# Kernel tuning notes

Measured on AMD Instinct MI355X. Metric: run time of the kernel, lower is better.

The kernel has to match this reference:

```python
import jax, jax.numpy as jnp
import numpy as np

LN_EPS = 1e-5


def layernorm(x, g, b):
    mu = jnp.mean(x, axis=-1, keepdims=True)
    var = jnp.mean((x - mu) ** 2, axis=-1, keepdims=True)
    return (x - mu) * jax.lax.rsqrt(var + LN_EPS) * g + b


def attention(x, qkv_w, proj_w, proj_b, num_heads):
    B, N, C = x.shape
    d = C // num_heads
    qkv = jnp.einsum('bnc,oc->bno', x, qkv_w)            # [B,N,3C], no bias (qkv_bias=False)
    qkv = qkv.reshape(B, N, num_heads, 3 * d).transpose(0, 2, 1, 3)  # [B,h,N,3d]
    q, k, v = qkv[..., :d], qkv[..., d:2 * d], qkv[..., 2 * d:]
    scores = jnp.einsum('bhnd,bhmd->bhnm', q, k) * (d ** -0.5)
    a = jax.nn.softmax(scores, axis=-1)
    o = jnp.einsum('bhnm,bhmd->bhnd', a, v).transpose(0, 2, 1, 3).reshape(B, N, C)
    return jnp.einsum('bnc,oc->bno', o, proj_w) + proj_b


def dwconv(x, w, b, H, W):
    # x: [B,N,C] -> NCHW depthwise 3x3 conv, stride 1, pad 1 -> [B,N,C]
    B, N, C = x.shape
    xi = x.transpose(0, 2, 1).reshape(B, C, H, W)
    y = jax.lax.conv_general_dilated(
        xi, w, window_strides=(1, 1), padding='SAME',
        dimension_numbers=('NCHW', 'OIHW', 'NCHW'), feature_group_count=C)
    y = y + b[None, :, None, None]
    return y.reshape(B, C, H * W).transpose(0, 2, 1)


def mlp(x, fc1_w, fc1_b, dw_w, dw_b, fc2_w, fc2_b, H, W):
    h = jnp.einsum('bnc,oc->bno', x, fc1_w) + fc1_b
    h = dwconv(h, dw_w, dw_b, H, W)
    h = jax.nn.gelu(h, approximate=False)  # torch nn.GELU default = exact erf
    return jnp.einsum('bnh,oh->bno', h, fc2_w) + fc2_b


def setup_inputs() -> dict:
    key = jax.random.key(0)
    ks = jax.random.split(key, 8)
    B, N, C, HID = 8, 1024, 512, 2048
    s = 0.02
    return {
        'x': jax.random.normal(ks[0], (B, N, C), jnp.float32),
        'ln1_g': jnp.ones((C,), jnp.float32),
        'ln1_b': jnp.zeros((C,), jnp.float32),
        'qkv_w': jax.random.normal(ks[1], (3 * C, C), jnp.float32) * s,
        'proj_w': jax.random.normal(ks[2], (C, C), jnp.float32) * s,
        'proj_b': jnp.zeros((C,), jnp.float32),
        'ln2_g': jnp.ones((C,), jnp.float32),
        'ln2_b': jnp.zeros((C,), jnp.float32),
        'fc1_w': jax.random.normal(ks[3], (HID, C), jnp.float32) * s,
        'fc1_b': jnp.zeros((HID,), jnp.float32),
        'dw_w': jax.random.normal(ks[4], (HID, 1, 3, 3), jnp.float32) * s,
        'dw_b': jnp.zeros((HID,), jnp.float32),
        'fc2_w': jax.random.normal(ks[5], (C, HID), jnp.float32) * s,
        'fc2_b': jnp.zeros((C,), jnp.float32),
        'H': 32,
        'W': 32,
    }


def reference(x, ln1_g, ln1_b, qkv_w, proj_w, proj_b, ln2_g, ln2_b,
              fc1_w, fc1_b, dw_w, dw_b, fc2_w, fc2_b, H, W):
    NUM_HEADS = 8
    x = x + attention(layernorm(x, ln1_g, ln1_b), qkv_w, proj_w, proj_b, NUM_HEADS)
    x = x + mlp(layernorm(x, ln2_g, ln2_b), fc1_w, fc1_b, dw_w, dw_b, fc2_w, fc2_b, H, W)
    return x
```

## Files before the change

kernel.cpp:

```cpp
#include <hip/hip_runtime.h>
#include <hip/hip_bf16.h>


typedef __attribute__((ext_vector_type(8))) short short8;
typedef __attribute__((ext_vector_type(4))) short s16x4;
typedef __attribute__((ext_vector_type(4))) float f32x4;

__device__ __forceinline__ float b2f(short s) {
    union { float f; unsigned u; } z; z.u = ((unsigned)(unsigned short)s) << 16; return z.f;
}
__device__ __forceinline__ short f2b(float f) {
    union { float f; unsigned u; } z; z.f = f;
    unsigned r = (z.u + 0x7fffu + ((z.u >> 16) & 1u)) >> 16;
    return (short)r;
}
__device__ __forceinline__ float erf_fast(float x) {
    float ax = fabsf(x);
    float t = 1.0f / fmaf(0.3275911f, ax, 1.0f);
    float p = t * fmaf(t, fmaf(t, fmaf(t, fmaf(t, 1.061405429f, -1.453152027f),
                        1.421413741f), -0.284496736f), 0.254829592f);
    float r = 1.0f - p * __expf(-ax * ax);
    return x < 0.f ? -r : r;
}

__device__ __forceinline__ void gload_lds16(const void* g, void* l) {
    __builtin_amdgcn_global_load_lds(
        (const __attribute__((address_space(1))) void*)g,
        (__attribute__((address_space(3))) void*)l, 16, 0, 0);
}

__global__ __launch_bounds__(256) void cvt_weights(
    const float* __restrict__ s0, const float* __restrict__ s1,
    const float* __restrict__ s2, const float* __restrict__ s3,
    short* __restrict__ d0, short* __restrict__ d1,
    short* __restrict__ d2, short* __restrict__ d3) {
    long i = (long)blockIdx.x * 256 + threadIdx.x;
    const float* s; short* d; long off;
    if (i < 196608)      { s = s0; d = d0; off = i; }
    else if (i < 262144) { s = s1; d = d1; off = i - 196608; }
    else if (i < 524288) { s = s2; d = d2; off = i - 262144; }
    else                 { s = s3; d = d3; off = i - 524288; }
    float4 v = ((const float4*)s)[off];
    ushort4 o;
    o.x = (unsigned short)f2b(v.x); o.y = (unsigned short)f2b(v.y);
    o.z = (unsigned short)f2b(v.z); o.w = (unsigned short)f2b(v.w);
    ((ushort4*)d)[off] = o;
}

__global__ __launch_bounds__(256) void cvt_dw(
    const float* __restrict__ src, float* __restrict__ dst) {
    int i = blockIdx.x * 256 + threadIdx.x;
    int t = i >> 11, c = i & 2047;
    dst[t * 2048 + c] = src[c * 9 + t];
}

__global__ __launch_bounds__(256) void ln_kernel(
    const float* __restrict__ x, const float* __restrict__ g,
    const float* __restrict__ b, short* __restrict__ y) {
    int row  = blockIdx.x * 4 + (threadIdx.x >> 6);
    int lane = threadIdx.x & 63;
    const float* xr = x + (long)row * 512 + lane * 8;
    float4 v0 = ((const float4*)xr)[0];
    float4 v1 = ((const float4*)xr)[1];
    float e0[8] = {v0.x, v0.y, v0.z, v0.w, v1.x, v1.y, v1.z, v1.w};
    float s = 0.f;
#pragma unroll
    for (int e = 0; e < 8; e++) s += e0[e];
#pragma unroll
    for (int d = 1; d < 64; d <<= 1) s += __shfl_xor(s, d);
    float mu = s * (1.0f / 512.0f);
    float q = 0.f;
#pragma unroll
    for (int e = 0; e < 8; e++) { float t = e0[e] - mu; q += t * t; }
#pragma unroll
    for (int d = 1; d < 64; d <<= 1) q += __shfl_xor(q, d);
    float rs = rsqrtf(q * (1.0f / 512.0f) + 1e-5f);
    const float* gp = g + lane * 8;
    const float* bp = b + lane * 8;
    short8 o;
#pragma unroll
    for (int e = 0; e < 8; e++) o[e] = f2b((e0[e] - mu) * rs * gp[e] + bp[e]);
    *(short8*)(y + (long)row * 512 + lane * 8) = o;
}

template <int MT, typename Epi>
__global__ __launch_bounds__(256, 4) void gemm_bt(
    const short* __restrict__ A, const short* __restrict__ B, int K, Epi epi) {
    constexpr int NJ = (MT == 128) ? 4 : 2;
    __shared__ short As[MT * 64];
    __shared__ short Bs[128 * 64];
    int tid = threadIdx.x;
    int lane = tid & 63, w = tid >> 6;
    int lr = lane & 15, lq = lane >> 4;
    int wm = (MT == 128) ? (w & 1) * 64 : 0;
    int wn = (MT == 128) ? (w >> 1) * 64 : w * 32;
    long r0 = (long)blockIdx.x * MT, o0 = (long)blockIdx.y * 128;
    f32x4 acc[4][NJ];
#pragma unroll
    for (int i = 0; i < 4; i++)
#pragma unroll
        for (int j = 0; j < NJ; j++) acc[i][j] = (f32x4){0.f, 0.f, 0.f, 0.f};
    const short* Ab = A + r0 * K;
    const short* Bb = B + o0 * K;
    int srow = tid >> 3;
    int sc = ((tid & 7) ^ (srow & 7)) * 8;
    for (int k0 = 0; k0 < K; k0 += 64) {
#pragma unroll
        for (int m = 0; m < MT / 32; m++)
            gload_lds16(Ab + (long)(srow + m * 32) * K + k0 + sc,
                        As + m * 2048 + w * 512);
#pragma unroll
        for (int m = 0; m < 4; m++)
            gload_lds16(Bb + (long)(srow + m * 32) * K + k0 + sc,
                        Bs + m * 2048 + w * 512);
        __syncthreads();
#pragma unroll
        for (int ks = 0; ks < 2; ks++) {
            short8 af[4], bfr[NJ];
#pragma unroll
            for (int i = 0; i < 4; i++) {
                int row = wm + i * 16 + lr;
                int c = ks * 4 + lq;
                af[i] = *(const short8*)&As[row * 64 + ((c ^ (row & 7)) * 8)];
            }
#pragma unroll
            for (int j = 0; j < NJ; j++) {
                int row = wn + j * 16 + lr;
                int c = ks * 4 + lq;
                bfr[j] = *(const short8*)&Bs[row * 64 + ((c ^ (row & 7)) * 8)];
            }
#pragma unroll
            for (int i = 0; i < 4; i++)
#pragma unroll
                for (int j = 0; j < NJ; j++)
                    acc[i][j] = __builtin_amdgcn_mfma_f32_16x16x32_bf16(
                        af[i], bfr[j], acc[i][j], 0, 0, 0);
        }
        __syncthreads();
    }
#pragma unroll
    for (int i = 0; i < 4; i++)
#pragma unroll
        for (int j = 0; j < NJ; j++)
#pragma unroll
            for (int rg = 0; rg < 4; rg++)
                epi((int)(r0 + wm + i * 16 + lq * 4 + rg),
                    (int)(o0 + wn + j * 16 + lr), acc[i][j][rg]);
}

struct EpiQKV {
    short *q, *k, *vt;
    __device__ void operator()(int r, int o, float v) const {
        int b = r >> 10, n = r & 1023;
        int h = o / 192, j = o - h * 192;
        int bh = b * 8 + h;
        short bv = f2b(v);
        if (j < 64)        q[((long)bh * 1024 + n) * 64 + j] = bv;
        else if (j < 128)  k[((long)bh * 1024 + n) * 64 + (j - 64)] = bv;
        else               vt[((long)bh * 64 + (j - 128)) * 1024 + n] = bv;
    }
};
struct EpiProj {
    const float* pb; const float* x; float* x1;
    __device__ void operator()(int r, int o, float v) const {
        long idx = (long)r * 512 + o;
        x1[idx] = v + pb[o] + x[idx];
    }
};
struct EpiBias {
    const float* bias; short* out; int O;
    __device__ void operator()(int r, int o, float v) const {
        out[(long)r * O + o] = f2b(v + bias[o]);
    }
};
struct EpiFc2 {
    const float* bias; const float* x1; float* out;
    __device__ void operator()(int r, int o, float v) const {
        long idx = (long)r * 512 + o;
        out[idx] = v + bias[o] + x1[idx];
    }
};

__global__ __launch_bounds__(256, 4) void attn_kernel(
    const short* __restrict__ Q, const short* __restrict__ K,
    const short* __restrict__ Vt, short* __restrict__ out) {
    __shared__ __align__(16) char smem[40960];
    int bh = blockIdx.x, qb = blockIdx.y;
    int tid = threadIdx.x, w = tid >> 6, lane = tid & 63;
    int lr = lane & 15, lq = lane >> 4;
    short* Pt = (short*)(smem + 32768) + w * 1024;

    const short* Qb = Q + ((long)bh * 1024 + qb * 64 + w * 16) * 64;
    const short* Kb = K + (long)bh * 1024 * 64;
    const short* Vb = Vt + (long)bh * 64 * 1024;

    int srow8 = lane >> 3, slot = lane & 7;

    short8 qf[2];
    qf[0] = *(const short8*)(Qb + lr * 64 + lq * 8);
    qf[1] = *(const short8*)(Qb + lr * 64 + 32 + lq * 8);

    f32x4 oacc[4];
#pragma unroll
    for (int dt = 0; dt < 4; dt++) oacc[dt] = (f32x4){0.f, 0.f, 0.f, 0.f};
    float lsum = 0.f;

#pragma unroll
    for (int m = 0; m < 2; m++) {
        int row = m * 32 + w * 8 + srow8;
        gload_lds16(Kb + (long)row * 64 + ((slot ^ (row & 7)) * 8),
                    (short*)smem + (m * 32 + w * 8) * 64);
        gload_lds16(Vb + (long)row * 1024 + ((slot ^ (row & 7)) * 8),
                    (short*)(smem + 16384) + (m * 32 + w * 8) * 64);
    }

    for (int it = 0; it < 16; it++) {
        __syncthreads();
        int cb = (it & 1) * 8192;
        if (it + 1 < 16) {
            int n0 = (it + 1) * 64, nb = ((it + 1) & 1) * 8192;
#pragma unroll
            for (int m = 0; m < 2; m++) {
                int row = m * 32 + w * 8 + srow8;
                gload_lds16(Kb + (long)(n0 + row) * 64 + ((slot ^ (row & 7)) * 8),
                            (short*)(smem + nb) + (m * 32 + w * 8) * 64);
                gload_lds16(Vb + (long)row * 1024 + n0 + ((slot ^ (row & 7)) * 8),
                            (short*)(smem + 16384 + nb) + (m * 32 + w * 8) * 64);
            }
        }
        const short* Kt = (const short*)(smem + cb);
        const short* Vl = (const short*)(smem + 16384 + cb);
        f32x4 sacc[4];
#pragma unroll
        for (int kt = 0; kt < 4; kt++) sacc[kt] = (f32x4){0.f, 0.f, 0.f, 0.f};
#pragma unroll
        for (int ks = 0; ks < 2; ks++)
#pragma unroll
            for (int kt = 0; kt < 4; kt++) {
                int row = kt * 16 + lr;
                short8 ak = *(const short8*)&Kt[row * 64 +
                                                (((ks * 4 + lq) ^ (row & 7)) * 8)];
                sacc[kt] = __builtin_amdgcn_mfma_f32_16x16x32_bf16(
                    ak, qf[ks], sacc[kt], 0, 0, 0);
            }
#pragma unroll
        for (int kt = 0; kt < 4; kt++) {
            float e0 = exp2f(sacc[kt][0] * 0.18033688f);
            float e1 = exp2f(sacc[kt][1] * 0.18033688f);
            float e2 = exp2f(sacc[kt][2] * 0.18033688f);
            float e3 = exp2f(sacc[kt][3] * 0.18033688f);
            lsum += (e0 + e1) + (e2 + e3);
            uint2 pk;
            pk.x = (__float_as_uint(e1) & 0xffff0000u) | (__float_as_uint(e0) >> 16);
            pk.y = (__float_as_uint(e3) & 0xffff0000u) | (__float_as_uint(e2) >> 16);
            int chunk = kt * 2 + (lq >> 1);
            *(uint2*)&Pt[lr * 64 + ((chunk ^ (lr & 7)) * 8) + (lq & 1) * 4] = pk;
        }
#pragma unroll
        for (int ks = 0; ks < 2; ks++) {
            short8 ap = *(const short8*)&Pt[lr * 64 +
                                            (((ks * 4 + lq) ^ (lr & 7)) * 8)];
#pragma unroll
            for (int dt = 0; dt < 4; dt++) {
                int row = dt * 16 + lr;
                short8 bv = *(const short8*)&Vl[row * 64 +
                                                (((ks * 4 + lq) ^ (row & 7)) * 8)];
                oacc[dt] = __builtin_amdgcn_mfma_f32_16x16x32_bf16(
                    ap, bv, oacc[dt], 0, 0, 0);
            }
        }
    }
    lsum += __shfl_xor(lsum, 16);
    lsum += __shfl_xor(lsum, 32);
    float inv = 1.0f / lsum;
    int b = bh >> 3, h = bh & 7;
    int qbase = qb * 64 + w * 16;
#pragma unroll
    for (int rg = 0; rg < 4; rg++) {
        float iv = __shfl(inv, lq * 4 + rg);
        long base = ((long)(b * 1024 + qbase + lq * 4 + rg)) * 512 + h * 64;
#pragma unroll
        for (int dt = 0; dt < 4; dt++)
            out[base + dt * 16 + lr] = f2b(oacc[dt][rg] * iv);
    }
}

__global__ __launch_bounds__(256, 3) void dwconv_gelu(
    const short* __restrict__ h1, const float* __restrict__ wdT,
    const float* __restrict__ bias, short* __restrict__ h2) {
    int ch = blockIdx.x & 1, xq = (blockIdx.x >> 1) & 3;
    int yy = (blockIdx.x >> 3) & 31, b = blockIdx.x >> 8;
    int c0 = ch * 1024 + threadIdx.x * 4;
    int x0 = xq * 8;
    float w[9][4];
#pragma unroll
    for (int t = 0; t < 9; t++) {
        float4 v = *(const float4*)&wdT[t * 2048 + c0];
        w[t][0] = v.x; w[t][1] = v.y; w[t][2] = v.z; w[t][3] = v.w;
    }
    float4 bv = *(const float4*)&bias[c0];
    float acc[8][4];
#pragma unroll
    for (int xi = 0; xi < 8; xi++) {
        acc[xi][0] = bv.x; acc[xi][1] = bv.y; acc[xi][2] = bv.z; acc[xi][3] = bv.w;
    }
#pragma unroll
    for (int ky = 0; ky < 3; ky++) {
        int ys = yy + ky - 1;
        if (ys < 0 || ys > 31) continue;
        const short* rp = h1 + ((long)(b * 1024 + ys * 32) * 2048 + c0);
        float fa[4], fb[4], fc[4];
        if (x0 > 0) {
            s16x4 v = *(const s16x4*)(rp + (long)(x0 - 1) * 2048);
#pragma unroll
            for (int e = 0; e < 4; e++) fa[e] = b2f(v[e]);
        } else {
#pragma unroll
            for (int e = 0; e < 4; e++) fa[e] = 0.f;
        }
        {
            s16x4 v = *(const s16x4*)(rp + (long)x0 * 2048);
#pragma unroll
            for (int e = 0; e < 4; e++) fb[e] = b2f(v[e]);
        }
#pragma unroll
        for (int xi = 0; xi < 8; xi++) {
            int xs = x0 + xi + 1;
            if (xs <= 31) {
                s16x4 v = *(const s16x4*)(rp + (long)xs * 2048);
#pragma unroll
                for (int e = 0; e < 4; e++) fc[e] = b2f(v[e]);
            } else {
#pragma unroll
                for (int e = 0; e < 4; e++) fc[e] = 0.f;
            }
#pragma unroll
            for (int e = 0; e < 4; e++)
                acc[xi][e] += fa[e] * w[ky * 3][e] + fb[e] * w[ky * 3 + 1][e] +
                              fc[e] * w[ky * 3 + 2][e];
#pragma unroll
            for (int e = 0; e < 4; e++) { fa[e] = fb[e]; fb[e] = fc[e]; }
        }
    }
#pragma unroll
    for (int xi = 0; xi < 8; xi++) {
        s16x4 o;
#pragma unroll
        for (int e = 0; e < 4; e++) {
            float a = acc[xi][e];
            o[e] = f2b(0.5f * a * (1.0f + erf_fast(a * 0.70710678118f)));
        }
        *(s16x4*)&h2[(long)(b * 1024 + yy * 32 + x0 + xi) * 2048 + c0] = o;
    }
}

extern "C" void kernel_launch(void* const* d_in, const int* in_sizes, int n_in,
                              void* d_out, int out_size, void* d_ws, size_t ws_size,
                              hipStream_t stream) {
    const float* x      = (const float*)d_in[0];
    const float* ln1_g  = (const float*)d_in[1];
    const float* ln1_b  = (const float*)d_in[2];
    const float* qkv_w  = (const float*)d_in[3];
    const float* proj_w = (const float*)d_in[4];
    const float* proj_b = (const float*)d_in[5];
    const float* ln2_g  = (const float*)d_in[6];
    const float* ln2_b  = (const float*)d_in[7];
    const float* fc1_w  = (const float*)d_in[8];
    const float* fc1_b  = (const float*)d_in[9];
    const float* dw_w   = (const float*)d_in[10];
    const float* dw_b   = (const float*)d_in[11];
    const float* fc2_w  = (const float*)d_in[12];
    const float* fc2_b  = (const float*)d_in[13];
    float* out = (float*)d_out;

    char* p = (char*)d_ws;
    short* wq   = (short*)p; p += (long)1536 * 512 * 2;
    short* wp   = (short*)p; p += (long)512 * 512 * 2;
    short* w1   = (short*)p; p += (long)2048 * 512 * 2;
    short* w2   = (short*)p; p += (long)512 * 2048 * 2;
    float* wdT  = (float*)p; p += (long)9 * 2048 * 4;
    short* y1   = (short*)p; p += (long)8192 * 512 * 2;
    short* q    = (short*)p; p += (long)64 * 1024 * 64 * 2;
    short* k    = (short*)p; p += (long)64 * 1024 * 64 * 2;
    short* vt   = (short*)p; p += (long)64 * 64 * 1024 * 2;
    short* attn = (short*)p; p += (long)8192 * 512 * 2;
    float* x1   = (float*)p; p += (long)8192 * 512 * 4;
    short* y2   = (short*)p; p += (long)8192 * 512 * 2;
    short* h1   = (short*)p; p += (long)8192 * 2048 * 2;
    short* h2   = (short*)p; p += (long)8192 * 2048 * 2;
    if ((size_t)(p - (char*)d_ws) > ws_size) return;

    cvt_weights<<<3072, 256, 0, stream>>>(qkv_w, proj_w, fc1_w, fc2_w, wq, wp, w1, w2);
    cvt_dw<<<72, 256, 0, stream>>>(dw_w, wdT);
    ln_kernel<<<2048, 256, 0, stream>>>(x, ln1_g, ln1_b, y1);
    gemm_bt<128><<<dim3(64, 12), 256, 0, stream>>>(y1, wq, 512, EpiQKV{q, k, vt});
    attn_kernel<<<dim3(64, 16), 256, 0, stream>>>(q, k, vt, attn);
    gemm_bt<64><<<dim3(128, 4), 256, 0, stream>>>(attn, wp, 512,
                                                  EpiProj{proj_b, x, x1});
    ln_kernel<<<2048, 256, 0, stream>>>(x1, ln2_g, ln2_b, y2);
    gemm_bt<128><<<dim3(64, 16), 256, 0, stream>>>(y2, w1, 512,
                                                   EpiBias{fc1_b, h1, 2048});
    dwconv_gelu<<<2048, 256, 0, stream>>>(h1, wdT, dw_b, h2);
    gemm_bt<64><<<dim3(128, 4), 256, 0, stream>>>(h2, w2, 2048,
                                                  EpiFc2{fc2_b, x1, out});
}
```

Measured before the change: 271.5 us.

## Double-buffer LDS tiles in gemm_bt and shrink K-tile to 32 for 128-row tiles

The GEMM main loop now keeps two LDS buffers, so the global-to-LDS loads for the next K-step are issued before the MFMAs on the current step. This is meant to hide global load latency and drops one barrier per iteration. For the 128-row variant the K-tile shrinks to 32 with a new XOR swizzle, which keeps the doubled LDS footprint the same as before and preserves occupancy. The cost is more loop iterations and barriers for that variant, and the 64-row variant doubles its LDS use, which may cut occupancy.

```diff
diff --git a/kernel.cpp b/kernel.cpp
--- a/kernel.cpp
+++ b/kernel.cpp
@@ -87,8 +87,10 @@
 __global__ __launch_bounds__(256, 4) void gemm_bt(
     const short* __restrict__ A, const short* __restrict__ B, int K, Epi epi) {
     constexpr int NJ = (MT == 128) ? 4 : 2;
-    __shared__ short As[MT * 64];
-    __shared__ short Bs[128 * 64];
+    constexpr int BK = (MT == 128) ? 32 : 64;
+    constexpr int RPR = (BK == 32) ? 64 : 32;
+    __shared__ short As[2][MT * BK];
+    __shared__ short Bs[2][128 * BK];
     int tid = threadIdx.x;
     int lane = tid & 63, w = tid >> 6;
     int lr = lane & 15, lq = lane >> 4;
@@ -102,32 +104,45 @@
         for (int j = 0; j < NJ; j++) acc[i][j] = (f32x4){0.f, 0.f, 0.f, 0.f};
     const short* Ab = A + r0 * K;
     const short* Bb = B + o0 * K;
-    int srow = tid >> 3;
-    int sc = ((tid & 7) ^ (srow & 7)) * 8;
-    for (int k0 = 0; k0 < K; k0 += 64) {
-#pragma unroll
-        for (int m = 0; m < MT / 32; m++)
-            gload_lds16(Ab + (long)(srow + m * 32) * K + k0 + sc,
-                        As + m * 2048 + w * 512);
-#pragma unroll
-        for (int m = 0; m < 4; m++)
-            gload_lds16(Bb + (long)(srow + m * 32) * K + k0 + sc,
-                        Bs + m * 2048 + w * 512);
+    int srow = (BK == 32) ? (tid >> 2) : (tid >> 3);
+    int sc = (BK == 32) ? (((tid & 3) ^ ((srow >> 1) & 3)) * 8)
+                        : (((tid & 7) ^ (srow & 7)) * 8);
+    int nsteps = K / BK;
+#pragma unroll
+    for (int m = 0; m < MT / RPR; m++)
+        gload_lds16(Ab + (long)(srow + m * RPR) * K + sc,
+                    &As[0][m * 2048 + w * 512]);
+#pragma unroll
+    for (int m = 0; m < 128 / RPR; m++)
+        gload_lds16(Bb + (long)(srow + m * RPR) * K + sc,
+                    &Bs[0][m * 2048 + w * 512]);
+    for (int s = 0; s < nsteps; s++) {
         __syncthreads();
-#pragma unroll
-        for (int ks = 0; ks < 2; ks++) {
+        int cb = s & 1;
+        if (s + 1 < nsteps) {
+            int k1 = (s + 1) * BK, nb = (s + 1) & 1;
+#pragma unroll
+            for (int m = 0; m < MT / RPR; m++)
+                gload_lds16(Ab + (long)(srow + m * RPR) * K + k1 + sc,
+                            &As[nb][m * 2048 + w * 512]);
+#pragma unroll
+            for (int m = 0; m < 128 / RPR; m++)
+                gload_lds16(Bb + (long)(srow + m * RPR) * K + k1 + sc,
+                            &Bs[nb][m * 2048 + w * 512]);
+        }
+        if constexpr (BK == 32) {
             short8 af[4], bfr[NJ];
 #pragma unroll
             for (int i = 0; i < 4; i++) {
                 int row = wm + i * 16 + lr;
-                int c = ks * 4 + lq;
-                af[i] = *(const short8*)&As[row * 64 + ((c ^ (row & 7)) * 8)];
+                af[i] = *(const short8*)&As[cb][row * 32 +
+                                               ((lq ^ ((row >> 1) & 3)) * 8)];
             }
 #pragma unroll
             for (int j = 0; j < NJ; j++) {
                 int row = wn + j * 16 + lr;
-                int c = ks * 4 + lq;
-                bfr[j] = *(const short8*)&Bs[row * 64 + ((c ^ (row & 7)) * 8)];
+                bfr[j] = *(const short8*)&Bs[cb][row * 32 +
+                                                 ((lq ^ ((row >> 1) & 3)) * 8)];
             }
 #pragma unroll
             for (int i = 0; i < 4; i++)
@@ -135,8 +150,32 @@
                 for (int j = 0; j < NJ; j++)
                     acc[i][j] = __builtin_amdgcn_mfma_f32_16x16x32_bf16(
                         af[i], bfr[j], acc[i][j], 0, 0, 0);
-        }
-        __syncthreads();
+        } else {
+#pragma unroll
+            for (int ks = 0; ks < 2; ks++) {
+                short8 af[4], bfr[NJ];
+#pragma unroll
+                for (int i = 0; i < 4; i++) {
+                    int row = wm + i * 16 + lr;
+                    int c = ks * 4 + lq;
+                    af[i] = *(const short8*)&As[cb][row * 64 +
+                                                    ((c ^ (row & 7)) * 8)];
+                }
+#pragma unroll
+                for (int j = 0; j < NJ; j++) {
+                    int row = wn + j * 16 + lr;
+                    int c = ks * 4 + lq;
+                    bfr[j] = *(const short8*)&Bs[cb][row * 64 +
+                                                     ((c ^ (row & 7)) * 8)];
+                }
+#pragma unroll
+                for (int i = 0; i < 4; i++)
+#pragma unroll
+                    for (int j = 0; j < NJ; j++)
+                        acc[i][j] = __builtin_amdgcn_mfma_f32_16x16x32_bf16(
+                            af[i], bfr[j], acc[i][j], 0, 0, 0);
+            }
+        }
     }
 #pragma unroll
     for (int i = 0; i < 4; i++)
```

Result: no change. 275.0 us (+1.3%).
